# Optimization experiments

Measured on AMD Instinct MI355X. Metric: run time of the kernel, lower is better.

## Reference

```python
import jax, jax.numpy as jnp
import numpy as np

B, S, E = 2, 2048, 1024
H, KV, D = 16, 4, 64
GC = 128          # ve_gate_channels
EPS = 1.1920929e-07  # torch F.rms_norm default eps for fp32
NEG = -1e30


def setup_inputs() -> dict:
    key = jax.random.key(0)
    ks = jax.random.split(key, 8)
    x = jax.random.normal(ks[0], (B, S, E), jnp.float32)
    ve = jax.random.normal(ks[1], (B, S, KV * D), jnp.float32)
    half = D // 2
    inv_freq = 1.0 / (10000.0 ** (np.arange(half, dtype=np.float64) / half))
    ang = np.arange(S, dtype=np.float64)[:, None] * inv_freq[None, :]
    cos = jnp.asarray(np.cos(ang), jnp.float32)[:, None, :]  # [S,1,D/2]
    sin = jnp.asarray(np.sin(ang), jnp.float32)[:, None, :]
    sc = E ** -0.5
    Wq = jax.random.normal(ks[2], (E, H * D), jnp.float32) * sc
    Wk = jax.random.normal(ks[3], (E, KV * D), jnp.float32) * sc
    Wv = jax.random.normal(ks[4], (E, KV * D), jnp.float32) * sc
    Wproj = jax.random.normal(ks[5], (E, E), jnp.float32) * sc
    Wgate = jax.random.normal(ks[6], (GC, KV), jnp.float32) * (GC ** -0.5)
    return {"x": x, "ve": ve, "cos": cos, "sin": sin, "Wq": Wq, "Wk": Wk,
            "Wv": Wv, "Wproj": Wproj, "Wgate": Wgate,
            "window_left": 1024, "window_right": 0}


def _rms(x):
    return x * jax.lax.rsqrt(jnp.mean(x * x, axis=-1, keepdims=True) + EPS)


def _rope(x, cos, sin):
    d = x.shape[-1] // 2
    x1, x2 = x[..., :d], x[..., d:]
    return jnp.concatenate([x1 * cos + x2 * sin, -x1 * sin + x2 * cos], axis=-1)


def reference(x, ve, cos, sin, Wq, Wk, Wv, Wproj, Wgate, window_left, window_right):
    b, s, e = x.shape
    q = (x @ Wq).reshape(b, s, H, D)
    k = (x @ Wk).reshape(b, s, KV, D)
    v = (x @ Wv).reshape(b, s, KV, D)
    # value-embedding gate: 2*sigmoid over first GC channels, per kv-head
    gate = 2.0 * jax.nn.sigmoid(x[..., :GC] @ Wgate)          # [B,S,KV]
    v = v + gate[..., None] * ve.reshape(b, s, KV, D)
    q = _rms(_rope(q, cos, sin))
    k = _rms(_rope(k, cos, sin))
    # GQA: repeat kv heads to match query heads
    g = H // KV
    kk = jnp.repeat(k, g, axis=2)                             # [B,S,H,D]
    vv = jnp.repeat(v, g, axis=2)
    scores = jnp.einsum('bihd,bjhd->bhij', q, kk) * (D ** -0.5)
    i = jnp.arange(s)[:, None]
    j = jnp.arange(s)[None, :]
    mask = (j <= i + window_right) & (j >= i - window_left) & (j <= i)
    scores = jnp.where(mask, scores, NEG)
    p = jax.nn.softmax(scores, axis=-1)
    y = jnp.einsum('bhij,bjhd->bihd', p, vv).reshape(b, s, H * D)
    return y @ Wproj
```

## Files before the change

### kernel.cpp

```cpp
#include <hip/hip_runtime.h>

typedef __bf16 bf16;
typedef __bf16 bf16x4 __attribute__((ext_vector_type(4)));
typedef __bf16 bf16x8 __attribute__((ext_vector_type(8)));
typedef float floatx4 __attribute__((ext_vector_type(4)));

#define EPS 1.1920929e-07f
#define QSCALE (0.125f * 1.44269504088896f)
#define SHIFT_C 11.5416f

__device__ __forceinline__ floatx4 mfma16(bf16x8 a, bf16x8 b, floatx4 c) {
  return __builtin_amdgcn_mfma_f32_16x16x32_bf16(a, b, c, 0, 0, 0);
}

__device__ __forceinline__ void gload16(const void* g, void* l) {
  __builtin_amdgcn_global_load_lds((const __attribute__((address_space(1))) unsigned int*)g,
                                   (__attribute__((address_space(3))) unsigned int*)l, 16, 0, 0);
}

__global__ void cast_x_kernel(const float* __restrict__ x, bf16* __restrict__ xb) {
  int i = (blockIdx.x * blockDim.x + threadIdx.x) * 4;
  float4 v = *(const float4*)(x + i);
  bf16x4 o = {(bf16)v.x, (bf16)v.y, (bf16)v.z, (bf16)v.w};
  *(bf16x4*)(xb + i) = o;
}

__global__ void pack_wqkv_kernel(const float* __restrict__ Wq, const float* __restrict__ Wk,
                                 const float* __restrict__ Wv, bf16* __restrict__ out) {
  __shared__ float tile[32][33];
  int n0 = blockIdx.x * 32, k0 = blockIdx.y * 32;
  int tx = threadIdx.x & 31, ty = threadIdx.x >> 5;
#pragma unroll
  for (int i = 0; i < 4; i++) {
    int k = k0 + ty + i * 8, n = n0 + tx;
    float v;
    if (n < 1024)      v = Wq[(size_t)k * 1024 + n];
    else if (n < 1280) v = Wk[(size_t)k * 256 + (n - 1024)];
    else               v = Wv[(size_t)k * 256 + (n - 1280)];
    tile[ty + i * 8][tx] = v;
  }
  __syncthreads();
#pragma unroll
  for (int i = 0; i < 4; i++) {
    int n = n0 + ty + i * 8, k = k0 + tx;
    out[(size_t)n * 1024 + k] = (bf16)tile[tx][ty + i * 8];
  }
}

__global__ void trans_wproj_kernel(const float* __restrict__ W, bf16* __restrict__ out) {
  __shared__ float tile[32][33];
  int n0 = blockIdx.x * 32, k0 = blockIdx.y * 32;
  int tx = threadIdx.x & 31, ty = threadIdx.x >> 5;
#pragma unroll
  for (int i = 0; i < 4; i++)
    tile[ty + i * 8][tx] = W[(size_t)(k0 + ty + i * 8) * 1024 + n0 + tx];
  __syncthreads();
#pragma unroll
  for (int i = 0; i < 4; i++)
    out[(size_t)(n0 + ty + i * 8) * 1024 + k0 + tx] = (bf16)tile[tx][ty + i * 8];
}

__global__ void gate_kernel(const float* __restrict__ x, const float* __restrict__ wgate,
                            float* __restrict__ gate) {
  int tid = blockIdx.x * 256 + threadIdx.x;
  int t = tid >> 2, kv = tid & 3;
  const float* xr = x + (size_t)t * 1024;
  float g = 0.f;
#pragma unroll 4
  for (int c = 0; c < 128; c++) g += xr[c] * wgate[c * 4 + kv];
  int b = t >> 11, s = t & 2047;
  gate[((size_t)b * 4 + kv) * 2048 + s] = 2.f / (1.f + __expf(-g));
}

__global__ __launch_bounds__(256) void qkv_gemm_kernel(const bf16* __restrict__ A,
                                                       const bf16* __restrict__ Bt,
                                                       const float* __restrict__ ve,
                                                       const float* __restrict__ cosb,
                                                       const float* __restrict__ sinb,
                                                       const float* __restrict__ gate,
                                                       bf16* __restrict__ Qb,
                                                       bf16* __restrict__ Kf,
                                                       bf16* __restrict__ Vf) {
  __shared__ __align__(16) char smem[24576];
  bf16* As = (bf16*)smem;
  bf16* Bs = (bf16*)(smem + 16384);
  bf16* Ep = (bf16*)smem;
  const int K = 1024;
  const int tid = threadIdx.x;
  const int tile = blockIdx.x;
  const int m0 = blockIdx.y * 128, n0 = tile * 64;
  const int w = tid >> 6, lane = tid & 63;
  const int q = lane >> 4, r0 = lane & 15;
  const int lrow = lane >> 2, lcol = (lane & 3) * 8;
  const int b = m0 >> 11, s0 = m0 & 2047;

  floatx4 acc[2][4];
#pragma unroll
  for (int i = 0; i < 2; i++)
#pragma unroll
    for (int j = 0; j < 4; j++) acc[i][j] = (floatx4){0.f, 0.f, 0.f, 0.f};

  for (int k0 = 0; k0 < K; k0 += 64) {
    __syncthreads();
#pragma unroll
    for (int i = 0; i < 4; i++) {
      int g = w * 4 + i, s = g >> 3, rb = g & 7;
      gload16(A + (size_t)(m0 + rb * 16 + lrow) * K + k0 + s * 32 + lcol, &As[s * 4096 + rb * 512]);
    }
#pragma unroll
    for (int i = 0; i < 2; i++) {
      int g = w * 2 + i, s = g >> 2, rb = g & 3;
      gload16(Bt + (size_t)(n0 + rb * 16 + lrow) * K + k0 + s * 32 + lcol, &Bs[s * 2048 + rb * 512]);
    }
    __syncthreads();
#pragma unroll
    for (int s = 0; s < 2; s++) {
      bf16x8 af[2], bfr[4];
#pragma unroll
      for (int mt = 0; mt < 2; mt++) af[mt] = *(const bf16x8*)&As[s * 4096 + (w * 32 + mt * 16 + r0) * 32 + q * 8];
#pragma unroll
      for (int nt = 0; nt < 4; nt++) bfr[nt] = *(const bf16x8*)&Bs[s * 2048 + (nt * 16 + r0) * 32 + q * 8];
#pragma unroll
      for (int mt = 0; mt < 2; mt++)
#pragma unroll
        for (int nt = 0; nt < 4; nt++)
          acc[mt][nt] = mfma16(af[mt], bfr[nt], acc[mt][nt]);
    }
  }
  __syncthreads();

  if (tile < 16) {
    const int h = tile;
#pragma unroll
    for (int mt = 0; mt < 2; mt++) {
      float rvv[4][4];
#pragma unroll
      for (int ntp = 0; ntp < 2; ntp++) {
        int d31 = ntp * 16 + r0;
#pragma unroll
        for (int r = 0; r < 4; r++) {
          int s = s0 + w * 32 + mt * 16 + q * 4 + r;
          float c = cosb[s * 32 + d31], sn = sinb[s * 32 + d31];
          float v1 = acc[mt][ntp][r], v2 = acc[mt][ntp + 2][r];
          rvv[ntp][r] = v1 * c + v2 * sn;
          rvv[ntp + 2][r] = v2 * c - v1 * sn;
        }
      }
#pragma unroll
      for (int r = 0; r < 4; r++) {
        float ss = 0.f;
#pragma unroll
        for (int nt = 0; nt < 4; nt++) ss += rvv[nt][r] * rvv[nt][r];
        ss += __shfl_xor(ss, 1, 64);
        ss += __shfl_xor(ss, 2, 64);
        ss += __shfl_xor(ss, 4, 64);
        ss += __shfl_xor(ss, 8, 64);
        float sc = rsqrtf(ss * (1.f / 64.f) + EPS) * QSCALE;
        int row = w * 32 + mt * 16 + q * 4 + r;
#pragma unroll
        for (int nt = 0; nt < 4; nt++)
          Ep[row * 72 + nt * 16 + r0] = (bf16)(rvv[nt][r] * sc);
      }
    }
    __syncthreads();
#pragma unroll
    for (int p = 0; p < 4; p++) {
      int g = p * 256 + tid;
      int row = g >> 3, chunk = g & 7;
      *(uint4*)&Qb[(((size_t)b * 16 + h) * 2048 + s0 + row) * 64 + chunk * 8] =
          *(const uint4*)&Ep[row * 72 + chunk * 8];
    }
  } else if (tile < 20) {
    const int kv = tile - 16;
#pragma unroll
    for (int mt = 0; mt < 2; mt++) {
      float rvv[4][4];
#pragma unroll
      for (int ntp = 0; ntp < 2; ntp++) {
        int d31 = ntp * 16 + r0;
#pragma unroll
        for (int r = 0; r < 4; r++) {
          int s = s0 + w * 32 + mt * 16 + q * 4 + r;
          float c = cosb[s * 32 + d31], sn = sinb[s * 32 + d31];
          float v1 = acc[mt][ntp][r], v2 = acc[mt][ntp + 2][r];
          rvv[ntp][r] = v1 * c + v2 * sn;
          rvv[ntp + 2][r] = v2 * c - v1 * sn;
        }
      }
#pragma unroll
      for (int r = 0; r < 4; r++) {
        float ss = 0.f;
#pragma unroll
        for (int nt = 0; nt < 4; nt++) ss += rvv[nt][r] * rvv[nt][r];
        ss += __shfl_xor(ss, 1, 64);
        ss += __shfl_xor(ss, 2, 64);
        ss += __shfl_xor(ss, 4, 64);
        ss += __shfl_xor(ss, 8, 64);
        float sc = rsqrtf(ss * (1.f / 64.f) + EPS);
        int row = w * 32 + mt * 16 + q * 4 + r;
#pragma unroll
        for (int nt = 0; nt < 4; nt++)
          Ep[row * 72 + nt * 16 + r0] = (bf16)(rvv[nt][r] * sc);
      }
    }
    __syncthreads();
    {
      int tk = (s0 >> 5) + w;
      size_t tb = ((size_t)(b * 4 + kv) * 64 + tk) * 2048;
#pragma unroll
      for (int u = 0; u < 4; u++) {
        int joff = (u >= 2) ? 16 : 0, doff = (u & 1) * 32;
        bf16x8 f = *(const bf16x8*)&Ep[(w * 32 + joff + r0) * 72 + doff + q * 8];
        *(bf16x8*)&Kf[tb + u * 512 + lane * 8] = f;
      }
    }
  } else {
    const int kv = tile - 20;
    const float* gbase = gate + ((size_t)b * 4 + kv) * 2048;
#pragma unroll
    for (int mt = 0; mt < 2; mt++) {
#pragma unroll
      for (int r = 0; r < 4; r++) {
        int row = w * 32 + mt * 16 + q * 4 + r;
        float gg = gbase[s0 + row];
#pragma unroll
        for (int nt = 0; nt < 4; nt++) {
          int d = nt * 16 + r0;
          float vv = acc[mt][nt][r] + gg * ve[(size_t)(m0 + row) * 256 + kv * 64 + d];
          Ep[row * 72 + d] = (bf16)vv;
        }
      }
    }
    __syncthreads();
    {
      int tk = (s0 >> 5) + w;
      size_t tb = ((size_t)(b * 4 + kv) * 64 + tk) * 2048;
#pragma unroll
      for (int nt = 0; nt < 4; nt++) {
        bf16 tmp[8];
#pragma unroll
        for (int e = 0; e < 8; e++) {
          int jl = w * 32 + (e >> 2) * 16 + 4 * q + (e & 3);
          tmp[e] = Ep[jl * 72 + nt * 16 + r0];
        }
        *(uint4*)&Vf[tb + nt * 512 + lane * 8] = *(uint4*)tmp;
      }
    }
  }
}

__global__ __launch_bounds__(256) void proj_gemm_kernel(const bf16* __restrict__ A,
                                                        const bf16* __restrict__ Bt,
                                                        float* __restrict__ Cout) {
  __shared__ __align__(16) bf16 As[2 * 128 * 32];
  __shared__ __align__(16) bf16 Bs[2 * 64 * 32];
  const int K = 1024, N = 1024;
  const int tid = threadIdx.x;
  const int m0 = blockIdx.y * 128, n0 = blockIdx.x * 64;
  const int w = tid >> 6, lane = tid & 63;
  const int q = lane >> 4, r0 = lane & 15;
  const int lrow = lane >> 2, lcol = (lane & 3) * 8;

  floatx4 acc[2][4];
#pragma unroll
  for (int i = 0; i < 2; i++)
#pragma unroll
    for (int j = 0; j < 4; j++) acc[i][j] = (floatx4){0.f, 0.f, 0.f, 0.f};

  for (int k0 = 0; k0 < K; k0 += 64) {
    __syncthreads();
#pragma unroll
    for (int i = 0; i < 4; i++) {
      int g = w * 4 + i, s = g >> 3, rb = g & 7;
      gload16(A + (size_t)(m0 + rb * 16 + lrow) * K + k0 + s * 32 + lcol, &As[s * 4096 + rb * 512]);
    }
#pragma unroll
    for (int i = 0; i < 2; i++) {
      int g = w * 2 + i, s = g >> 2, rb = g & 3;
      gload16(Bt + (size_t)(n0 + rb * 16 + lrow) * K + k0 + s * 32 + lcol, &Bs[s * 2048 + rb * 512]);
    }
    __syncthreads();
#pragma unroll
    for (int s = 0; s < 2; s++) {
      bf16x8 af[2], bfr[4];
#pragma unroll
      for (int mt = 0; mt < 2; mt++) af[mt] = *(const bf16x8*)&As[s * 4096 + (w * 32 + mt * 16 + r0) * 32 + q * 8];
#pragma unroll
      for (int nt = 0; nt < 4; nt++) bfr[nt] = *(const bf16x8*)&Bs[s * 2048 + (nt * 16 + r0) * 32 + q * 8];
#pragma unroll
      for (int mt = 0; mt < 2; mt++)
#pragma unroll
        for (int nt = 0; nt < 4; nt++)
          acc[mt][nt] = mfma16(af[mt], bfr[nt], acc[mt][nt]);
    }
  }
#pragma unroll
  for (int mt = 0; mt < 2; mt++)
#pragma unroll
    for (int nt = 0; nt < 4; nt++)
#pragma unroll
      for (int r = 0; r < 4; r++) {
        int row = m0 + w * 32 + mt * 16 + q * 4 + r;
        int col = n0 + nt * 16 + r0;
        Cout[(size_t)row * N + col] = acc[mt][nt][r];
      }
}

__global__ __launch_bounds__(512, 4) void attn_kernel(const bf16* __restrict__ Qb,
                                                      const bf16* __restrict__ Kf,
                                                      const bf16* __restrict__ Vf,
                                                      const int* __restrict__ wlp,
                                                      const int* __restrict__ wrp,
                                                      bf16* __restrict__ Yb) {
  __shared__ float Ol[4 * 64 * 21];
  const int wl = wlp[0];
  const int wrc = min(wrp[0], 0);
  const int blk = blockIdx.x;
  const int lo = blk & 31, hi = blk >> 5;
  const int qc = (lo + hi * 9) & 31;
  const int bh = hi;
  const int b = bh >> 4, h = bh & 15, kvh = (bh & 15) >> 2;
  const int w = threadIdx.x >> 6, lane = threadIdx.x & 63;
  const int wq = w & 3, jh = w >> 2;
  const int q = lane >> 4, r0 = lane & 15;
  const int q0 = qc * 64 + wq * 16;

  const bf16* qbase = Qb + (((size_t)b * 16 + h) * 2048 + q0 + r0) * 64;
  bf16x8 aq0 = *(const bf16x8*)(qbase + q * 8);
  bf16x8 aq1 = *(const bf16x8*)(qbase + 32 + q * 8);

  floatx4 Oacc[4];
#pragma unroll
  for (int nt = 0; nt < 4; nt++) Oacc[nt] = (floatx4){0.f, 0.f, 0.f, 0.f};
  floatx4 Lacc = (floatx4){0.f, 0.f, 0.f, 0.f};

  const bf16 onev = (bf16)1.0f;
  const bf16x8 ones = {onev, onev, onev, onev, onev, onev, onev, onev};

  const int jlo0 = max(0, q0 - wl) & ~31;
  const int jhi = q0 + 15 + wrc;
  const int n = ((jhi - jlo0) >> 5) + 1;
  const int nlo = (n + 1) >> 1;
  const int jstart = jh ? jlo0 + (nlo << 5) : jlo0;
  const int count = jh ? n - nlo : nlo;

  const bf16* kfb = Kf + ((size_t)(b * 4 + kvh) * 64) * 2048 + lane * 8;
  const bf16* vfb = Vf + ((size_t)(b * 4 + kvh) * 64) * 2048 + lane * 8;

  if (count > 0) {
    int tile0 = jstart >> 5;
    bf16x8 kf[4], vf[4], nk[4], nv[4];
#pragma unroll
    for (int u = 0; u < 4; u++) {
      kf[u] = *(const bf16x8*)(kfb + (size_t)tile0 * 2048 + u * 512);
      vf[u] = *(const bf16x8*)(vfb + (size_t)tile0 * 2048 + u * 512);
    }

    for (int t = 0; t < count; t++) {
      const int j0 = jstart + (t << 5);
      const int tn = (t + 1 < count) ? tile0 + t + 1 : tile0 + t;
#pragma unroll
      for (int u = 0; u < 4; u++) {
        nk[u] = *(const bf16x8*)(kfb + (size_t)tn * 2048 + u * 512);
        nv[u] = *(const bf16x8*)(vfb + (size_t)tn * 2048 + u * 512);
      }

      floatx4 s0 = (floatx4){-SHIFT_C, -SHIFT_C, -SHIFT_C, -SHIFT_C};
      floatx4 s1 = s0;
      s0 = mfma16(kf[0], aq0, s0);
      s0 = mfma16(kf[1], aq1, s0);
      s1 = mfma16(kf[2], aq0, s1);
      s1 = mfma16(kf[3], aq1, s1);

      bf16x8 pa;
      if (j0 >= q0 + 15 - wl && j0 + 31 <= q0 + wrc) {
#pragma unroll
        for (int r = 0; r < 4; r++) {
          pa[r] = (bf16)exp2f(s0[r]);
          pa[4 + r] = (bf16)exp2f(s1[r]);
        }
      } else {
        const int i = q0 + r0;
#pragma unroll
        for (int r = 0; r < 4; r++) {
          int ja = j0 + 4 * q + r, jb = ja + 16;
          bool va = (ja <= i + wrc) && (ja >= i - wl);
          bool vb = (jb <= i + wrc) && (jb >= i - wl);
          pa[r] = va ? (bf16)exp2f(s0[r]) : (bf16)0.f;
          pa[4 + r] = vb ? (bf16)exp2f(s1[r]) : (bf16)0.f;
        }
      }

      Lacc = mfma16(pa, ones, Lacc);
#pragma unroll
      for (int nt = 0; nt < 4; nt++) Oacc[nt] = mfma16(pa, vf[nt], Oacc[nt]);

#pragma unroll
      for (int u = 0; u < 4; u++) { kf[u] = nk[u]; vf[u] = nv[u]; }
    }
  }

  float* mbase = Ol + (wq * 64 + lane) * 21;
  if (jh == 1) {
#pragma unroll
    for (int nt = 0; nt < 4; nt++)
#pragma unroll
      for (int r = 0; r < 4; r++) mbase[nt * 4 + r] = Oacc[nt][r];
#pragma unroll
    for (int r = 0; r < 4; r++) mbase[16 + r] = Lacc[r];
  }
  __syncthreads();
  if (jh == 0) {
    float inv[4];
#pragma unroll
    for (int r = 0; r < 4; r++) inv[r] = 1.f / (Lacc[r] + mbase[16 + r]);
#pragma unroll
    for (int nt = 0; nt < 4; nt++)
#pragma unroll
      for (int r = 0; r < 4; r++) {
        int i = q0 + q * 4 + r;
        float o = (Oacc[nt][r] + mbase[nt * 4 + r]) * inv[r];
        Yb[((size_t)b * 2048 + i) * 1024 + h * 64 + nt * 16 + r0] = (bf16)o;
      }
  }
}

extern "C" void kernel_launch(void* const* d_in, const int* in_sizes, int n_in,
                              void* d_out, int out_size, void* d_ws, size_t ws_size,
                              hipStream_t stream) {
  const float* x     = (const float*)d_in[0];
  const float* ve    = (const float*)d_in[1];
  const float* cosb  = (const float*)d_in[2];
  const float* sinb  = (const float*)d_in[3];
  const float* Wq    = (const float*)d_in[4];
  const float* Wk    = (const float*)d_in[5];
  const float* Wv    = (const float*)d_in[6];
  const float* Wproj = (const float*)d_in[7];
  const float* Wgate = (const float*)d_in[8];
  const int* wl      = (const int*)d_in[9];
  const int* wr      = (const int*)d_in[10];

  char* ws = (char*)d_ws;
  bf16* Xb      = (bf16*)(ws);
  bf16* Wqkv_t  = (bf16*)(ws + 8388608);
  bf16* Wproj_t = (bf16*)(ws + 11534336);
  bf16* Qb      = (bf16*)(ws + 13631488);
  bf16* Kf      = (bf16*)(ws + 22020096);
  bf16* Vf      = (bf16*)(ws + 24117248);
  bf16* Yb      = (bf16*)(ws + 26214400);
  float* gateb  = (float*)(ws + 34603008);

  cast_x_kernel<<<4096, 256, 0, stream>>>(x, Xb);
  pack_wqkv_kernel<<<dim3(48, 32), 256, 0, stream>>>(Wq, Wk, Wv, Wqkv_t);
  trans_wproj_kernel<<<dim3(32, 32), 256, 0, stream>>>(Wproj, Wproj_t);
  gate_kernel<<<64, 256, 0, stream>>>(x, Wgate, gateb);
  qkv_gemm_kernel<<<dim3(24, 32), 256, 0, stream>>>(Xb, Wqkv_t, ve, cosb, sinb, gateb, Qb, Kf, Vf);
  attn_kernel<<<1024, 512, 0, stream>>>(Qb, Kf, Vf, wl, wr, Yb);
  proj_gemm_kernel<<<dim3(16, 32), 256, 0, stream>>>(Yb, Wproj_t, (float*)d_out);
}
```

Baseline: 182.4 us.

## Process two query tiles per wave sharing K/V loads, drop split-KV merge

Each wave now handles 32 query rows (two 16-row MFMA tiles) over the full key range, so each loaded K/V fragment feeds twice as many MFMAs. The key-range split across two wave halves, its LDS merge and __syncthreads are removed. Query chunks are paired (p, 31-p, 32+p, 63-p) across the four waves of a block to balance causal work. Launch changes to 512 blocks of 256 threads. This trades fewer waves and longer serial loops per wave, plus higher register pressure, for less K/V traffic and no cross-wave reduction.

```diff
diff --git a/kernel.cpp b/kernel.cpp
--- a/kernel.cpp
+++ b/kernel.cpp
@@ -306,123 +306,139 @@
       }
 }
 
-__global__ __launch_bounds__(512, 4) void attn_kernel(const bf16* __restrict__ Qb,
+__global__ __launch_bounds__(256, 2) void attn_kernel(const bf16* __restrict__ Qb,
                                                       const bf16* __restrict__ Kf,
                                                       const bf16* __restrict__ Vf,
                                                       const int* __restrict__ wlp,
                                                       const int* __restrict__ wrp,
                                                       bf16* __restrict__ Yb) {
-  __shared__ float Ol[4 * 64 * 21];
   const int wl = wlp[0];
   const int wrc = min(wrp[0], 0);
   const int blk = blockIdx.x;
-  const int lo = blk & 31, hi = blk >> 5;
-  const int qc = (lo + hi * 9) & 31;
-  const int bh = hi;
+  const int p = blk & 15, bh = blk >> 4;
   const int b = bh >> 4, h = bh & 15, kvh = (bh & 15) >> 2;
   const int w = threadIdx.x >> 6, lane = threadIdx.x & 63;
-  const int wq = w & 3, jh = w >> 2;
   const int q = lane >> 4, r0 = lane & 15;
-  const int q0 = qc * 64 + wq * 16;
-
-  const bf16* qbase = Qb + (((size_t)b * 16 + h) * 2048 + q0 + r0) * 64;
-  bf16x8 aq0 = *(const bf16x8*)(qbase + q * 8);
-  bf16x8 aq1 = *(const bf16x8*)(qbase + 32 + q * 8);
-
-  floatx4 Oacc[4];
-#pragma unroll
-  for (int nt = 0; nt < 4; nt++) Oacc[nt] = (floatx4){0.f, 0.f, 0.f, 0.f};
-  floatx4 Lacc = (floatx4){0.f, 0.f, 0.f, 0.f};
+  const int cm = (w == 0) ? p : (w == 1) ? 31 - p : (w == 2) ? 32 + p : 63 - p;
+  const int q0 = cm * 32;
+  const int qA = q0, qB = q0 + 16;
+
+  const bf16* qbase = Qb + (((size_t)b * 16 + h) * 2048 + qA + r0) * 64;
+  bf16x8 aqA0 = *(const bf16x8*)(qbase + q * 8);
+  bf16x8 aqA1 = *(const bf16x8*)(qbase + 32 + q * 8);
+  bf16x8 aqB0 = *(const bf16x8*)(qbase + 16 * 64 + q * 8);
+  bf16x8 aqB1 = *(const bf16x8*)(qbase + 16 * 64 + 32 + q * 8);
+
+  floatx4 OA[4], OB[4];
+#pragma unroll
+  for (int nt = 0; nt < 4; nt++) {
+    OA[nt] = (floatx4){0.f, 0.f, 0.f, 0.f};
+    OB[nt] = (floatx4){0.f, 0.f, 0.f, 0.f};
+  }
+  floatx4 LA = (floatx4){0.f, 0.f, 0.f, 0.f};
+  floatx4 LB = LA;
 
   const bf16 onev = (bf16)1.0f;
   const bf16x8 ones = {onev, onev, onev, onev, onev, onev, onev, onev};
 
-  const int jlo0 = max(0, q0 - wl) & ~31;
-  const int jhi = q0 + 15 + wrc;
-  const int n = ((jhi - jlo0) >> 5) + 1;
-  const int nlo = (n + 1) >> 1;
-  const int jstart = jh ? jlo0 + (nlo << 5) : jlo0;
-  const int count = jh ? n - nlo : nlo;
+  const int jlo = max(0, q0 - wl) & ~31;
+  const int jhi = q0 + 31 + wrc;
+  const int count = ((jhi - jlo) >> 5) + 1;
+  const int tile0 = jlo >> 5;
 
   const bf16* kfb = Kf + ((size_t)(b * 4 + kvh) * 64) * 2048 + lane * 8;
   const bf16* vfb = Vf + ((size_t)(b * 4 + kvh) * 64) * 2048 + lane * 8;
 
-  if (count > 0) {
-    int tile0 = jstart >> 5;
-    bf16x8 kf[4], vf[4], nk[4], nv[4];
+  bf16x8 kf[4], vf[4], nk[4], nv[4];
+#pragma unroll
+  for (int u = 0; u < 4; u++) {
+    kf[u] = *(const bf16x8*)(kfb + (size_t)tile0 * 2048 + u * 512);
+    vf[u] = *(const bf16x8*)(vfb + (size_t)tile0 * 2048 + u * 512);
+  }
+
+  for (int t = 0; t < count; t++) {
+    const int j0 = jlo + (t << 5);
+    const int tn = (t + 1 < count) ? tile0 + t + 1 : tile0 + t;
 #pragma unroll
     for (int u = 0; u < 4; u++) {
-      kf[u] = *(const bf16x8*)(kfb + (size_t)tile0 * 2048 + u * 512);
-      vf[u] = *(const bf16x8*)(vfb + (size_t)tile0 * 2048 + u * 512);
-    }
-
-    for (int t = 0; t < count; t++) {
-      const int j0 = jstart + (t << 5);
-      const int tn = (t + 1 < count) ? tile0 + t + 1 : tile0 + t;
-#pragma unroll
-      for (int u = 0; u < 4; u++) {
-        nk[u] = *(const bf16x8*)(kfb + (size_t)tn * 2048 + u * 512);
-        nv[u] = *(const bf16x8*)(vfb + (size_t)tn * 2048 + u * 512);
-      }
-
-      floatx4 s0 = (floatx4){-SHIFT_C, -SHIFT_C, -SHIFT_C, -SHIFT_C};
-      floatx4 s1 = s0;
-      s0 = mfma16(kf[0], aq0, s0);
-      s0 = mfma16(kf[1], aq1, s0);
-      s1 = mfma16(kf[2], aq0, s1);
-      s1 = mfma16(kf[3], aq1, s1);
-
-      bf16x8 pa;
-      if (j0 >= q0 + 15 - wl && j0 + 31 <= q0 + wrc) {
-#pragma unroll
-        for (int r = 0; r < 4; r++) {
-          pa[r] = (bf16)exp2f(s0[r]);
-          pa[4 + r] = (bf16)exp2f(s1[r]);
-        }
-      } else {
-        const int i = q0 + r0;
-#pragma unroll
-        for (int r = 0; r < 4; r++) {
-          int ja = j0 + 4 * q + r, jb = ja + 16;
-          bool va = (ja <= i + wrc) && (ja >= i - wl);
-          bool vb = (jb <= i + wrc) && (jb >= i - wl);
-          pa[r] = va ? (bf16)exp2f(s0[r]) : (bf16)0.f;
-          pa[4 + r] = vb ? (bf16)exp2f(s1[r]) : (bf16)0.f;
-        }
-      }
-
-      Lacc = mfma16(pa, ones, Lacc);
-#pragma unroll
-      for (int nt = 0; nt < 4; nt++) Oacc[nt] = mfma16(pa, vf[nt], Oacc[nt]);
-
-#pragma unroll
-      for (int u = 0; u < 4; u++) { kf[u] = nk[u]; vf[u] = nv[u]; }
-    }
-  }
-
-  float* mbase = Ol + (wq * 64 + lane) * 21;
-  if (jh == 1) {
-#pragma unroll
-    for (int nt = 0; nt < 4; nt++)
-#pragma unroll
-      for (int r = 0; r < 4; r++) mbase[nt * 4 + r] = Oacc[nt][r];
-#pragma unroll
-    for (int r = 0; r < 4; r++) mbase[16 + r] = Lacc[r];
-  }
-  __syncthreads();
-  if (jh == 0) {
-    float inv[4];
-#pragma unroll
-    for (int r = 0; r < 4; r++) inv[r] = 1.f / (Lacc[r] + mbase[16 + r]);
-#pragma unroll
-    for (int nt = 0; nt < 4; nt++)
-#pragma unroll
-      for (int r = 0; r < 4; r++) {
-        int i = q0 + q * 4 + r;
-        float o = (Oacc[nt][r] + mbase[nt * 4 + r]) * inv[r];
-        Yb[((size_t)b * 2048 + i) * 1024 + h * 64 + nt * 16 + r0] = (bf16)o;
-      }
-  }
+      nk[u] = *(const bf16x8*)(kfb + (size_t)tn * 2048 + u * 512);
+      nv[u] = *(const bf16x8*)(vfb + (size_t)tn * 2048 + u * 512);
+    }
+
+    floatx4 sA0 = (floatx4){-SHIFT_C, -SHIFT_C, -SHIFT_C, -SHIFT_C};
+    floatx4 sA1 = sA0, sB0 = sA0, sB1 = sA0;
+    sA0 = mfma16(kf[0], aqA0, sA0);
+    sA0 = mfma16(kf[1], aqA1, sA0);
+    sA1 = mfma16(kf[2], aqA0, sA1);
+    sA1 = mfma16(kf[3], aqA1, sA1);
+    sB0 = mfma16(kf[0], aqB0, sB0);
+    sB0 = mfma16(kf[1], aqB1, sB0);
+    sB1 = mfma16(kf[2], aqB0, sB1);
+    sB1 = mfma16(kf[3], aqB1, sB1);
+
+    bf16x8 paA, paB;
+    if (j0 >= qA + 15 - wl && j0 + 31 <= qA + wrc) {
+#pragma unroll
+      for (int r = 0; r < 4; r++) {
+        paA[r] = (bf16)exp2f(sA0[r]);
+        paA[4 + r] = (bf16)exp2f(sA1[r]);
+      }
+    } else {
+      const int i = qA + r0;
+#pragma unroll
+      for (int r = 0; r < 4; r++) {
+        int ja = j0 + 4 * q + r, jb = ja + 16;
+        bool va = (ja <= i + wrc) && (ja >= i - wl);
+        bool vb = (jb <= i + wrc) && (jb >= i - wl);
+        paA[r] = va ? (bf16)exp2f(sA0[r]) : (bf16)0.f;
+        paA[4 + r] = vb ? (bf16)exp2f(sA1[r]) : (bf16)0.f;
+      }
+    }
+    if (j0 >= qB + 15 - wl && j0 + 31 <= qB + wrc) {
+#pragma unroll
+      for (int r = 0; r < 4; r++) {
+        paB[r] = (bf16)exp2f(sB0[r]);
+        paB[4 + r] = (bf16)exp2f(sB1[r]);
+      }
+    } else {
+      const int i = qB + r0;
+#pragma unroll
+      for (int r = 0; r < 4; r++) {
+        int ja = j0 + 4 * q + r, jb = ja + 16;
+        bool va = (ja <= i + wrc) && (ja >= i - wl);
+        bool vb = (jb <= i + wrc) && (jb >= i - wl);
+        paB[r] = va ? (bf16)exp2f(sB0[r]) : (bf16)0.f;
+        paB[4 + r] = vb ? (bf16)exp2f(sB1[r]) : (bf16)0.f;
+      }
+    }
+
+    LA = mfma16(paA, ones, LA);
+    LB = mfma16(paB, ones, LB);
+#pragma unroll
+    for (int nt = 0; nt < 4; nt++) {
+      OA[nt] = mfma16(paA, vf[nt], OA[nt]);
+      OB[nt] = mfma16(paB, vf[nt], OB[nt]);
+    }
+
+#pragma unroll
+    for (int u = 0; u < 4; u++) { kf[u] = nk[u]; vf[u] = nv[u]; }
+  }
+
+  float invA[4], invB[4];
+#pragma unroll
+  for (int r = 0; r < 4; r++) {
+    invA[r] = 1.f / LA[r];
+    invB[r] = 1.f / LB[r];
+  }
+#pragma unroll
+  for (int nt = 0; nt < 4; nt++)
+#pragma unroll
+    for (int r = 0; r < 4; r++) {
+      int iA = qA + q * 4 + r;
+      Yb[((size_t)b * 2048 + iA) * 1024 + h * 64 + nt * 16 + r0] = (bf16)(OA[nt][r] * invA[r]);
+      int iB = qB + q * 4 + r;
+      Yb[((size_t)b * 2048 + iB) * 1024 + h * 64 + nt * 16 + r0] = (bf16)(OB[nt][r] * invB[r]);
+    }
 }
 
 extern "C" void kernel_launch(void* const* d_in, const int* in_sizes, int n_in,
@@ -455,6 +471,6 @@
   trans_wproj_kernel<<<dim3(32, 32), 256, 0, stream>>>(Wproj, Wproj_t);
   gate_kernel<<<64, 256, 0, stream>>>(x, Wgate, gateb);
   qkv_gemm_kernel<<<dim3(24, 32), 256, 0, stream>>>(Xb, Wqkv_t, ve, cosb, sinb, gateb, Qb, Kf, Vf);
-  attn_kernel<<<1024, 512, 0, stream>>>(Qb, Kf, Vf, wl, wr, Yb);
+  attn_kernel<<<512, 256, 0, stream>>>(Qb, Kf, Vf, wl, wr, Yb);
   proj_gemm_kernel<<<dim3(16, 32), 256, 0, stream>>>(Yb, Wproj_t, (float*)d_out);
 }
```

Result: no change. 179.4 us (-1.6%).
